# Kernel tuning notes

Hardware: AMD Instinct MI355X
Metric: run time of the kernel (lower is better)

## Reference

```python
import jax, jax.numpy as jnp
import numpy as np

B, N, D = 4, 2048, 4
COUPLING = 1.0
DT = 1.0


def setup_inputs() -> dict:
    key = jax.random.key(0)
    k1, k2, k3, k4 = jax.random.split(key, 4)
    theta_prev = jax.random.normal(k1, (B, N, D), dtype=jnp.float32)
    gamma_t = jax.random.normal(k2, (B, N, D), dtype=jnp.float32)
    affinity = jax.random.uniform(k3, (B, N, N), dtype=jnp.float32)
    alpha_t = jax.random.normal(k4, (B, N, N), dtype=jnp.float32)
    # learned parameters, initialized as in the torch module
    omega = jnp.zeros((N, D), dtype=jnp.float32)
    kappa = jnp.ones((N, D), dtype=jnp.float32)
    alpha_bias = jnp.zeros((N, N), dtype=jnp.float32)
    return {
        "theta_prev": theta_prev,
        "gamma_t": gamma_t,
        "affinity": affinity,
        "alpha_t": alpha_t,
        "omega": omega,
        "kappa": kappa,
        "alpha_bias": alpha_bias,
    }


def reference(theta_prev, gamma_t, affinity, alpha_t, omega, kappa, alpha_bias):
    # theta_prev: [B, N, D], affinity/alpha_t: [B, N, N]
    n = theta_prev.shape[1]
    alpha_total = alpha_t + alpha_bias[None, :, :]               # [B, N, N]
    # phase_term[b, i, j, d] = sin(theta[b, j, d] - theta[b, i, d] - alpha_total[b, i, j])
    phase_term = jnp.sin(
        theta_prev[:, None, :, :] - theta_prev[:, :, None, :]
        - alpha_total[:, :, :, None]
    )                                                            # [B, N, N, D]
    coupling_term = (COUPLING / n) * jnp.einsum(
        "bij,bijd->bid", affinity, phase_term
    )                                                            # [B, N, D]
    drive_term = kappa[None, :, :] * (gamma_t - theta_prev)
    theta_dot = omega[None, :, :] + drive_term + coupling_term
    return theta_prev + DT * theta_dot
```

## Files before the change

kernel.cpp:

```cpp
#include <hip/hip_runtime.h>

#define BB 4
#define NN 2048
#define DD 4
#define ROWS 2
#define BLOCK 256
#define QPT 4
#define JITER (NN / (BLOCK * QPT))

typedef float f4 __attribute__((ext_vector_type(4)));

__global__ __launch_bounds__(BLOCK) void sincos_theta(const float* __restrict__ theta,
                                                      float* __restrict__ sArr,
                                                      float* __restrict__ cArr) {
    const int idx = blockIdx.x * BLOCK + threadIdx.x;
    const float x = theta[idx];
    float s, c;
    __sincosf(x, &s, &c);
    sArr[idx] = s;
    cArr[idx] = c;
}

__global__ __launch_bounds__(BLOCK) void kuramoto_main(
    const float* __restrict__ theta,
    const float* __restrict__ gam,
    const float* __restrict__ aff,
    const float* __restrict__ alp,
    const float* __restrict__ omega,
    const float* __restrict__ kappa,
    const float* __restrict__ bias,
    const float* __restrict__ sArr,
    const float* __restrict__ cArr,
    float* __restrict__ out)
{
    const int tid = threadIdx.x;
    const int blk = blockIdx.x;
    const int rowBlocks = NN / ROWS;
    const int b  = blk / rowBlocks;
    const int i0 = (blk % rowBlocks) * ROWS;

    const f4* __restrict__ aff4 = (const f4*)(aff + (size_t)b * NN * NN);
    const f4* __restrict__ alp4 = (const f4*)(alp + (size_t)b * NN * NN);
    const f4* __restrict__ bia4 = (const f4*)bias;
    const f4* __restrict__ s4   = (const f4*)sArr + (size_t)b * NN;
    const f4* __restrict__ c4   = (const f4*)cArr + (size_t)b * NN;

    float accU[ROWS][DD];
    float accV[ROWS][DD];
    #pragma unroll
    for (int r = 0; r < ROWS; ++r)
        #pragma unroll
        for (int d = 0; d < DD; ++d) { accU[r][d] = 0.f; accV[r][d] = 0.f; }

    #pragma unroll
    for (int jj = 0; jj < JITER; ++jj) {
        const int q  = jj * BLOCK + tid;
        const int j0 = q * QPT;

        f4 av[ROWS], lv[ROWS], bv[ROWS];
        #pragma unroll
        for (int r = 0; r < ROWS; ++r) {
            const size_t qo = (size_t)(i0 + r) * (NN / QPT) + q;
            av[r] = __builtin_nontemporal_load(&aff4[qo]);
            lv[r] = __builtin_nontemporal_load(&alp4[qo]);
            bv[r] = bia4[qo];
        }
        f4 sj[QPT], cj[QPT];
        #pragma unroll
        for (int u = 0; u < QPT; ++u) { sj[u] = s4[j0 + u]; cj[u] = c4[j0 + u]; }

        #pragma unroll
        for (int r = 0; r < ROWS; ++r) {
            const f4 alr = lv[r] + bv[r];
            const float aA[4] = {av[r].x, av[r].y, av[r].z, av[r].w};
            const float lA[4] = {alr.x, alr.y, alr.z, alr.w};
            #pragma unroll
            for (int u = 0; u < QPT; ++u) {
                float sa, ca;
                __sincosf(lA[u], &sa, &ca);
                const float wc = aA[u] * ca;
                const float ws = aA[u] * sa;
                accU[r][0] = fmaf(wc, sj[u].x, fmaf(-ws, cj[u].x, accU[r][0]));
                accU[r][1] = fmaf(wc, sj[u].y, fmaf(-ws, cj[u].y, accU[r][1]));
                accU[r][2] = fmaf(wc, sj[u].z, fmaf(-ws, cj[u].z, accU[r][2]));
                accU[r][3] = fmaf(wc, sj[u].w, fmaf(-ws, cj[u].w, accU[r][3]));
                accV[r][0] = fmaf(wc, cj[u].x, fmaf(ws, sj[u].x, accV[r][0]));
                accV[r][1] = fmaf(wc, cj[u].y, fmaf(ws, sj[u].y, accV[r][1]));
                accV[r][2] = fmaf(wc, cj[u].z, fmaf(ws, sj[u].z, accV[r][2]));
                accV[r][3] = fmaf(wc, cj[u].w, fmaf(ws, sj[u].w, accV[r][3]));
            }
        }
    }

    __shared__ float red[BLOCK / 64][ROWS * 2 * DD];
    const int wave = tid >> 6;
    const int lane = tid & 63;

    #pragma unroll
    for (int r = 0; r < ROWS; ++r) {
        #pragma unroll
        for (int d = 0; d < DD; ++d) {
            float u = accU[r][d];
            float v = accV[r][d];
            #pragma unroll
            for (int off = 32; off >= 1; off >>= 1) {
                u += __shfl_down(u, off, 64);
                v += __shfl_down(v, off, 64);
            }
            if (lane == 0) {
                red[wave][r * 2 * DD + d]      = u;
                red[wave][r * 2 * DD + DD + d] = v;
            }
        }
    }
    __syncthreads();

    if (tid < ROWS * DD) {
        const int r = tid >> 2;
        const int d = tid & 3;
        float U = 0.f, V = 0.f;
        #pragma unroll
        for (int w = 0; w < BLOCK / 64; ++w) {
            U += red[w][r * 2 * DD + d];
            V += red[w][r * 2 * DD + DD + d];
        }
        const int i = i0 + r;
        const int idx = (b * NN + i) * DD + d;
        const float s_i = sArr[idx];
        const float c_i = cArr[idx];
        const float coup = (1.0f / (float)NN) * (c_i * U - s_i * V);
        const float th = theta[idx];
        const float o  = omega[i * DD + d];
        const float k  = kappa[i * DD + d];
        out[idx] = th + o + k * (gam[idx] - th) + coup;
    }
}

extern "C" void kernel_launch(void* const* d_in, const int* in_sizes, int n_in,
                              void* d_out, int out_size, void* d_ws, size_t ws_size,
                              hipStream_t stream) {
    const float* theta = (const float*)d_in[0];
    const float* gam   = (const float*)d_in[1];
    const float* aff   = (const float*)d_in[2];
    const float* alp   = (const float*)d_in[3];
    const float* omega = (const float*)d_in[4];
    const float* kappa = (const float*)d_in[5];
    const float* bias  = (const float*)d_in[6];
    float* out  = (float*)d_out;

    float* sArr = (float*)d_ws;
    float* cArr = sArr + BB * NN * DD;

    sincos_theta<<<(BB * NN * DD) / BLOCK, BLOCK, 0, stream>>>(theta, sArr, cArr);
    kuramoto_main<<<(BB * NN) / ROWS, BLOCK, 0, stream>>>(
        theta, gam, aff, alp, omega, kappa, bias, sArr, cArr, out);
}
```

Baseline: 178.2 us.

## Assign row pairs per wave, pack sin/cos in fp16, prefetch and interleave batches

Each wave now owns two rows and sweeps all columns, so the cross-wave shared-memory reduction and block barrier go away. The per-column sin/cos of theta are stored a second time as packed fp16 in a d-major layout, which halves that traffic and gives one 16-byte load per d. Loads of affinity, alpha and bias are double-buffered one iteration ahead, and block indices are interleaved across batches so that concurrent blocks share bias rows. Using fp16 for sin/cos adds rounding error to the coupling sum.

Result: faster. 173.2 us (-2.8%).

```diff
diff --git a/kernel.cpp b/kernel.cpp
--- a/kernel.cpp
+++ b/kernel.cpp
@@ -3,22 +3,49 @@
 #define BB 4
 #define NN 2048
 #define DD 4
-#define ROWS 2
+#define QQ (NN / 4)
 #define BLOCK 256
-#define QPT 4
-#define JITER (NN / (BLOCK * QPT))
+#define JIT (QQ / 64)
 
 typedef float f4 __attribute__((ext_vector_type(4)));
-
-__global__ __launch_bounds__(BLOCK) void sincos_theta(const float* __restrict__ theta,
-                                                      float* __restrict__ sArr,
-                                                      float* __restrict__ cArr) {
-    const int idx = blockIdx.x * BLOCK + threadIdx.x;
-    const float x = theta[idx];
-    float s, c;
-    __sincosf(x, &s, &c);
-    sArr[idx] = s;
-    cArr[idx] = c;
+typedef _Float16 h8 __attribute__((ext_vector_type(8)));
+
+__global__ __launch_bounds__(BLOCK) void precomp(const float* __restrict__ theta,
+                                                 float* __restrict__ sArr,
+                                                 float* __restrict__ cArr,
+                                                 h8* __restrict__ scT) {
+    const int t = blockIdx.x * BLOCK + threadIdx.x;
+    const int b = t / QQ, q = t % QQ;
+    const f4* theta4 = (const f4*)theta;
+    f4* s4 = (f4*)sArr;
+    f4* c4 = (f4*)cArr;
+
+    float s[4][4], c[4][4];
+    #pragma unroll
+    for (int u = 0; u < 4; ++u) {
+        const f4 th = theta4[(size_t)b * NN + 4 * q + u];
+        const float thA[4] = {th.x, th.y, th.z, th.w};
+        #pragma unroll
+        for (int d = 0; d < 4; ++d) __sincosf(thA[d], &s[u][d], &c[u][d]);
+    }
+    #pragma unroll
+    for (int u = 0; u < 4; ++u) {
+        f4 sv, cv;
+        sv.x = s[u][0]; sv.y = s[u][1]; sv.z = s[u][2]; sv.w = s[u][3];
+        cv.x = c[u][0]; cv.y = c[u][1]; cv.z = c[u][2]; cv.w = c[u][3];
+        s4[(size_t)b * NN + 4 * q + u] = sv;
+        c4[(size_t)b * NN + 4 * q + u] = cv;
+    }
+    #pragma unroll
+    for (int d = 0; d < 4; ++d) {
+        h8 w;
+        #pragma unroll
+        for (int u = 0; u < 4; ++u) {
+            w[2 * u]     = (_Float16)s[u][d];
+            w[2 * u + 1] = (_Float16)c[u][d];
+        }
+        scT[((size_t)b * 4 + d) * QQ + q] = w;
+    }
 }
 
 __global__ __launch_bounds__(BLOCK) void kuramoto_main(
@@ -31,108 +58,138 @@
     const float* __restrict__ bias,
     const float* __restrict__ sArr,
     const float* __restrict__ cArr,
+    const h8* __restrict__ scT,
     float* __restrict__ out)
 {
-    const int tid = threadIdx.x;
-    const int blk = blockIdx.x;
-    const int rowBlocks = NN / ROWS;
-    const int b  = blk / rowBlocks;
-    const int i0 = (blk % rowBlocks) * ROWS;
-
-    const f4* __restrict__ aff4 = (const f4*)(aff + (size_t)b * NN * NN);
-    const f4* __restrict__ alp4 = (const f4*)(alp + (size_t)b * NN * NN);
-    const f4* __restrict__ bia4 = (const f4*)bias;
-    const f4* __restrict__ s4   = (const f4*)sArr + (size_t)b * NN;
-    const f4* __restrict__ c4   = (const f4*)cArr + (size_t)b * NN;
-
-    float accU[ROWS][DD];
-    float accV[ROWS][DD];
-    #pragma unroll
-    for (int r = 0; r < ROWS; ++r)
-        #pragma unroll
-        for (int d = 0; d < DD; ++d) { accU[r][d] = 0.f; accV[r][d] = 0.f; }
-
-    #pragma unroll
-    for (int jj = 0; jj < JITER; ++jj) {
-        const int q  = jj * BLOCK + tid;
-        const int j0 = q * QPT;
-
-        f4 av[ROWS], lv[ROWS], bv[ROWS];
-        #pragma unroll
-        for (int r = 0; r < ROWS; ++r) {
-            const size_t qo = (size_t)(i0 + r) * (NN / QPT) + q;
-            av[r] = __builtin_nontemporal_load(&aff4[qo]);
-            lv[r] = __builtin_nontemporal_load(&alp4[qo]);
-            bv[r] = bia4[qo];
-        }
-        f4 sj[QPT], cj[QPT];
-        #pragma unroll
-        for (int u = 0; u < QPT; ++u) { sj[u] = s4[j0 + u]; cj[u] = c4[j0 + u]; }
-
-        #pragma unroll
-        for (int r = 0; r < ROWS; ++r) {
-            const f4 alr = lv[r] + bv[r];
-            const float aA[4] = {av[r].x, av[r].y, av[r].z, av[r].w};
+    const int x   = blockIdx.x;
+    const int low = x & 31;
+    const int b   = low >> 3;
+    const int g   = (x >> 5) * 8 + (low & 7);
+    const int i0  = g * 8;
+
+    const int tid  = threadIdx.x;
+    const int wave = tid >> 6;
+    const int lane = tid & 63;
+    const int r0   = i0 + 2 * wave;
+
+    const f4* aff4 = (const f4*)(aff + (size_t)b * NN * NN);
+    const f4* alp4 = (const f4*)(alp + (size_t)b * NN * NN);
+    const f4* bia4 = (const f4*)bias;
+    const h8* scb  = scT + (size_t)b * 4 * QQ;
+
+    float accU[2][4], accV[2][4];
+    #pragma unroll
+    for (int r = 0; r < 2; ++r)
+        #pragma unroll
+        for (int d = 0; d < 4; ++d) { accU[r][d] = 0.f; accV[r][d] = 0.f; }
+
+    f4 av[2][2], lv[2][2], bv[2][2];
+    {
+        const int q = lane;
+        #pragma unroll
+        for (int r = 0; r < 2; ++r) {
+            const size_t qo = (size_t)(r0 + r) * QQ + q;
+            av[0][r] = __builtin_nontemporal_load(&aff4[qo]);
+            lv[0][r] = __builtin_nontemporal_load(&alp4[qo]);
+            bv[0][r] = bia4[qo];
+        }
+    }
+
+    #pragma unroll
+    for (int jj = 0; jj < JIT; ++jj) {
+        const int cur = jj & 1;
+        const int nxt = cur ^ 1;
+        const int q   = lane + 64 * jj;
+
+        if (jj + 1 < JIT) {
+            const int qn = lane + 64 * (jj + 1);
+            #pragma unroll
+            for (int r = 0; r < 2; ++r) {
+                const size_t qo = (size_t)(r0 + r) * QQ + qn;
+                av[nxt][r] = __builtin_nontemporal_load(&aff4[qo]);
+                lv[nxt][r] = __builtin_nontemporal_load(&alp4[qo]);
+                bv[nxt][r] = bia4[qo];
+            }
+        }
+
+        float sj[4][4], cj[4][4];
+        #pragma unroll
+        for (int d = 0; d < 4; ++d) {
+            const h8 w = scb[(size_t)d * QQ + q];
+            #pragma unroll
+            for (int u = 0; u < 4; ++u) {
+                sj[u][d] = (float)w[2 * u];
+                cj[u][d] = (float)w[2 * u + 1];
+            }
+        }
+
+        #pragma unroll
+        for (int r = 0; r < 2; ++r) {
+            const f4 alr = lv[cur][r] + bv[cur][r];
+            const float aA[4] = {av[cur][r].x, av[cur][r].y, av[cur][r].z, av[cur][r].w};
             const float lA[4] = {alr.x, alr.y, alr.z, alr.w};
             #pragma unroll
-            for (int u = 0; u < QPT; ++u) {
+            for (int u = 0; u < 4; ++u) {
                 float sa, ca;
                 __sincosf(lA[u], &sa, &ca);
                 const float wc = aA[u] * ca;
                 const float ws = aA[u] * sa;
-                accU[r][0] = fmaf(wc, sj[u].x, fmaf(-ws, cj[u].x, accU[r][0]));
-                accU[r][1] = fmaf(wc, sj[u].y, fmaf(-ws, cj[u].y, accU[r][1]));
-                accU[r][2] = fmaf(wc, sj[u].z, fmaf(-ws, cj[u].z, accU[r][2]));
-                accU[r][3] = fmaf(wc, sj[u].w, fmaf(-ws, cj[u].w, accU[r][3]));
-                accV[r][0] = fmaf(wc, cj[u].x, fmaf(ws, sj[u].x, accV[r][0]));
-                accV[r][1] = fmaf(wc, cj[u].y, fmaf(ws, sj[u].y, accV[r][1]));
-                accV[r][2] = fmaf(wc, cj[u].z, fmaf(ws, sj[u].z, accV[r][2]));
-                accV[r][3] = fmaf(wc, cj[u].w, fmaf(ws, sj[u].w, accV[r][3]));
-            }
-        }
-    }
-
-    __shared__ float red[BLOCK / 64][ROWS * 2 * DD];
-    const int wave = tid >> 6;
-    const int lane = tid & 63;
-
-    #pragma unroll
-    for (int r = 0; r < ROWS; ++r) {
-        #pragma unroll
-        for (int d = 0; d < DD; ++d) {
-            float u = accU[r][d];
-            float v = accV[r][d];
+                #pragma unroll
+                for (int d = 0; d < 4; ++d) {
+                    accU[r][d] = fmaf(wc, sj[u][d], fmaf(-ws, cj[u][d], accU[r][d]));
+                    accV[r][d] = fmaf(wc, cj[u][d], fmaf(ws, sj[u][d], accV[r][d]));
+                }
+            }
+        }
+    }
+
+    #pragma unroll
+    for (int r = 0; r < 2; ++r)
+        #pragma unroll
+        for (int d = 0; d < 4; ++d) {
+            float u = accU[r][d], v = accV[r][d];
             #pragma unroll
             for (int off = 32; off >= 1; off >>= 1) {
                 u += __shfl_down(u, off, 64);
                 v += __shfl_down(v, off, 64);
             }
-            if (lane == 0) {
-                red[wave][r * 2 * DD + d]      = u;
-                red[wave][r * 2 * DD + DD + d] = v;
-            }
-        }
-    }
-    __syncthreads();
-
-    if (tid < ROWS * DD) {
-        const int r = tid >> 2;
-        const int d = tid & 3;
-        float U = 0.f, V = 0.f;
-        #pragma unroll
-        for (int w = 0; w < BLOCK / 64; ++w) {
-            U += red[w][r * 2 * DD + d];
-            V += red[w][r * 2 * DD + DD + d];
-        }
-        const int i = i0 + r;
-        const int idx = (b * NN + i) * DD + d;
-        const float s_i = sArr[idx];
-        const float c_i = cArr[idx];
-        const float coup = (1.0f / (float)NN) * (c_i * U - s_i * V);
-        const float th = theta[idx];
-        const float o  = omega[i * DD + d];
-        const float k  = kappa[i * DD + d];
-        out[idx] = th + o + k * (gam[idx] - th) + coup;
+            accU[r][d] = u; accV[r][d] = v;
+        }
+
+    if (lane == 0) {
+        const f4* theta4 = (const f4*)theta;
+        const f4* gam4   = (const f4*)gam;
+        const f4* om4    = (const f4*)omega;
+        const f4* kp4    = (const f4*)kappa;
+        const f4* s4     = (const f4*)sArr;
+        const f4* c4     = (const f4*)cArr;
+        f4* out4         = (f4*)out;
+        #pragma unroll
+        for (int r = 0; r < 2; ++r) {
+            const int i = r0 + r;
+            const size_t base = (size_t)b * NN + i;
+            const f4 th = theta4[base];
+            const f4 gm = gam4[base];
+            const f4 om = om4[i];
+            const f4 kp = kp4[i];
+            const f4 si = s4[base];
+            const f4 ci = c4[base];
+            const float siA[4] = {si.x, si.y, si.z, si.w};
+            const float ciA[4] = {ci.x, ci.y, ci.z, ci.w};
+            const float thA[4] = {th.x, th.y, th.z, th.w};
+            const float gmA[4] = {gm.x, gm.y, gm.z, gm.w};
+            const float omA[4] = {om.x, om.y, om.z, om.w};
+            const float kpA[4] = {kp.x, kp.y, kp.z, kp.w};
+            f4 o;
+            float oA[4];
+            #pragma unroll
+            for (int d = 0; d < 4; ++d) {
+                const float coup = (1.0f / (float)NN) * (ciA[d] * accU[r][d] - siA[d] * accV[r][d]);
+                oA[d] = thA[d] + omA[d] + kpA[d] * (gmA[d] - thA[d]) + coup;
+            }
+            o.x = oA[0]; o.y = oA[1]; o.z = oA[2]; o.w = oA[3];
+            out4[base] = o;
+        }
     }
 }
 
@@ -150,8 +207,9 @@
 
     float* sArr = (float*)d_ws;
     float* cArr = sArr + BB * NN * DD;
-
-    sincos_theta<<<(BB * NN * DD) / BLOCK, BLOCK, 0, stream>>>(theta, sArr, cArr);
-    kuramoto_main<<<(BB * NN) / ROWS, BLOCK, 0, stream>>>(
-        theta, gam, aff, alp, omega, kappa, bias, sArr, cArr, out);
+    h8*    scT  = (h8*)(cArr + BB * NN * DD);
+
+    precomp<<<(BB * QQ) / BLOCK, BLOCK, 0, stream>>>(theta, sArr, cArr, scT);
+    kuramoto_main<<<BB * (NN / 8), BLOCK, 0, stream>>>(
+        theta, gam, aff, alp, omega, kappa, bias, sArr, cArr, scT, out);
 }
```
